# Kernel optimization log

Hardware: AMD Instinct MI355X
Metric: run time of the kernel (lower is better)

## Reference

```python
import jax, jax.numpy as jnp
import numpy as np

GAMMA = 0.997
N_STEPS = 5
EPS = 1e-3
Q_WEIGHTS = np.array([1.0, 0.5, 0.0, 2.0], dtype=np.float32)


def _rescale(x):
    # sign(x) * (sqrt(|x|+1) - 1) + eps * x
    return jnp.sign(x) * (jnp.sqrt(jnp.abs(x) + 1.0) - 1.0) + EPS * x


def _inv_rescale(x):
    sign = jnp.sign(x)
    sqrt_arg = 1.0 + 4.0 * EPS * (jnp.abs(x) + 1.0 + EPS)
    square = ((jnp.sqrt(sqrt_arg) - 1.0) / (2.0 * EPS)) ** 2
    return sign * (square - 1.0)


def setup_inputs() -> dict:
    key = jax.random.key(0)
    ks = jax.random.split(key, 6)
    B, T, Q = 4096, 512, 4
    current_q_value = jax.random.normal(ks[0], (B, T, Q), dtype=jnp.float32)
    next_q_value = jax.random.normal(ks[1], (B, T, Q), dtype=jnp.float32)
    log_p = jax.random.normal(ks[2], (B, T), dtype=jnp.float32)
    reward = jax.random.normal(ks[3], (B, T, Q), dtype=jnp.float32)
    is_done = jax.random.bernoulli(ks[4], 0.02, (B, T)).astype(jnp.float32)
    mask = jax.random.bernoulli(ks[5], 0.95, (B, T)).astype(jnp.float32)
    return {
        "current_q_value": current_q_value,
        "next_q_value": next_q_value,
        "log_p": log_p,
        "reward": reward,
        "is_done": is_done,
        "mask": mask,
    }


def reference(current_q_value, next_q_value, log_p, reward, is_done, mask):
    B, T, Q = reward.shape
    q_w = jnp.asarray(Q_WEIGHTS)[None, None, :]                     # (1,1,Q)
    nz = (q_w != 0)
    inv_qw = jnp.where(nz, 1.0 / jnp.where(nz, q_w, 1.0), 0.0)      # (1,1,Q)
    inv_num_q = 1.0 / float((Q_WEIGHTS != 0).sum())

    m = mask[..., None]                                             # (B,T,1)
    d = is_done[..., None]                                          # (B,T,1)

    nq = m * (1.0 - d) * _inv_rescale(next_q_value)                 # (B,T,Q)
    lp = inv_num_q * inv_qw * (m * (1.0 - d) * log_p[..., None])    # (B,T,Q)

    pad = jnp.zeros((B, N_STEPS - 1, Q), dtype=reward.dtype)
    pad_reward = jnp.concatenate([m * reward, pad], axis=1)         # (B,T+n-1,Q)
    lp_pad = jnp.concatenate([lp, pad], axis=1)                     # (B,T+n-1,Q)

    gpow = GAMMA ** jnp.arange(N_STEPS, dtype=jnp.float32)          # gamma^0..gamma^{n-1}
    widx = jnp.arange(T)[:, None] + jnp.arange(N_STEPS)[None, :]    # (T,n) window indices

    reward_sum = jnp.einsum('btnq,n->btq', pad_reward[:, widx, :], gpow)
    log_p_sum = jnp.einsum('btnq,n->btq', lp_pad[:, widx, :], gpow * GAMMA)

    idxs = jnp.minimum(T - 1, jnp.arange(T) + N_STEPS - 1)          # (T,)
    # NOTE: original code uses gamma**idx (absolute index), reproduced faithfully
    next_term = (GAMMA ** idxs.astype(jnp.float32))[None, :, None] * nq[:, idxs, :]

    target = _rescale(reward_sum + next_term + log_p_sum)           # (B,T,Q)
    loss = 0.5 * m * q_w * (current_q_value - target) ** 2
    return loss
```

## Files before the change

kernel.cpp:

```cpp
#include <hip/hip_runtime.h>
#include <math.h>

#define T_DIM 512
#define GAMMA_F 0.997f
#define EPS_F 1e-3f
#define LOG2_GAMMA (-0.0043345907f)

typedef float v4f __attribute__((ext_vector_type(4)));

__device__ __forceinline__ float inv_rescale_f(float x) {
    float s = (x > 0.f) ? 1.f : ((x < 0.f) ? -1.f : 0.f);
    float sqrt_arg = 1.f + 4.f * EPS_F * (fabsf(x) + 1.f + EPS_F);
    float q = (sqrtf(sqrt_arg) - 1.f) * (1.f / (2.f * EPS_F));
    return s * (q * q - 1.f);
}

__device__ __forceinline__ float rescale_f(float x) {
    return copysignf(sqrtf(fabsf(x) + 1.f) - 1.f, x) + EPS_F * x;
}

__global__ __launch_bounds__(256) void nstep_qloss_kernel(
    const float* __restrict__ cur_q,
    const float* __restrict__ next_q,
    const float* __restrict__ log_p,
    const float* __restrict__ reward,
    const float* __restrict__ is_done,
    const float* __restrict__ mask,
    float* __restrict__ out,
    int BT)
{
    int idx = blockIdx.x * 256 + threadIdx.x;
    if (idx >= BT) return;
    int t = idx & (T_DIM - 1);
    int base = idx - t;

    int s1 = (t + 1 < T_DIM) ? t + 1 : T_DIM - 1;
    int s2 = (t + 2 < T_DIM) ? t + 2 : T_DIM - 1;
    int s3 = (t + 3 < T_DIM) ? t + 3 : T_DIM - 1;
    int s4 = (t + 4 < T_DIM) ? t + 4 : T_DIM - 1;
    int o0 = idx;
    int o1 = base + s1, o2 = base + s2, o3 = base + s3, o4 = base + s4;

    const v4f* rew4 = (const v4f*)reward;
    const v4f* nq4  = (const v4f*)next_q;
    const v4f* cq4  = (const v4f*)cur_q;
    v4f* out4       = (v4f*)out;

    float m0 = mask[o0], m1 = mask[o1], m2 = mask[o2], m3 = mask[o3], m4 = mask[o4];
    float d0 = is_done[o0], d1 = is_done[o1], d2 = is_done[o2], d3 = is_done[o3], d4 = is_done[o4];
    float p0 = log_p[o0], p1 = log_p[o1], p2 = log_p[o2], p3 = log_p[o3], p4 = log_p[o4];
    v4f r0 = rew4[o0], r1 = rew4[o1], r2 = rew4[o2], r3 = rew4[o3], r4 = rew4[o4];
    v4f nq = nq4[o4];
    v4f cq = cq4[o0];

    float v1 = (t + 1 < T_DIM) ? 1.f : 0.f;
    float v2 = (t + 2 < T_DIM) ? 1.f : 0.f;
    float v3 = (t + 3 < T_DIM) ? 1.f : 0.f;
    float v4v = (t + 4 < T_DIM) ? 1.f : 0.f;

    const float g1 = GAMMA_F;
    const float g2 = g1 * g1;
    const float g3 = g2 * g1;
    const float g4 = g2 * g2;

    float w0 = m0;
    float w1 = v1 * g1 * m1;
    float w2 = v2 * g2 * m2;
    float w3 = v3 * g3 * m3;
    float w4 = v4v * g4 * m4;

    float a0 = w0 * r0.x; float a1 = w0 * r0.y; float a2 = w0 * r0.z; float a3 = w0 * r0.w;
    a0 = fmaf(w1, r1.x, a0); a1 = fmaf(w1, r1.y, a1); a2 = fmaf(w1, r1.z, a2); a3 = fmaf(w1, r1.w, a3);
    a0 = fmaf(w2, r2.x, a0); a1 = fmaf(w2, r2.y, a1); a2 = fmaf(w2, r2.z, a2); a3 = fmaf(w2, r2.w, a3);
    a0 = fmaf(w3, r3.x, a0); a1 = fmaf(w3, r3.y, a1); a2 = fmaf(w3, r3.z, a2); a3 = fmaf(w3, r3.w, a3);
    a0 = fmaf(w4, r4.x, a0); a1 = fmaf(w4, r4.y, a1); a2 = fmaf(w4, r4.z, a2); a3 = fmaf(w4, r4.w, a3);

    float Ls = w0 * (1.f - d0) * p0;
    Ls = fmaf(w1, (1.f - d1) * p1, Ls);
    Ls = fmaf(w2, (1.f - d2) * p2, Ls);
    Ls = fmaf(w3, (1.f - d3) * p3, Ls);
    Ls = fmaf(w4, (1.f - d4) * p4, Ls);
    Ls *= GAMMA_F * (1.f / 3.f);

    float coeff = exp2f((float)s4 * LOG2_GAMMA);
    float g = coeff * m4 * (1.f - d4);
    float nt0 = g * inv_rescale_f(nq.x);
    float nt1 = g * inv_rescale_f(nq.y);
    float nt2 = g * inv_rescale_f(nq.z);
    float nt3 = g * inv_rescale_f(nq.w);

    float tgt0 = rescale_f(a0 + nt0 + 1.0f * Ls);
    float tgt1 = rescale_f(a1 + nt1 + 2.0f * Ls);
    float tgt2 = rescale_f(a2 + nt2);
    float tgt3 = rescale_f(a3 + nt3 + 0.5f * Ls);

    float hm = 0.5f * m0;
    float e0 = cq.x - tgt0;
    float e1 = cq.y - tgt1;
    float e3 = cq.w - tgt3;
    (void)tgt2;
    v4f o;
    o.x = hm * e0 * e0;
    o.y = hm * 0.5f * e1 * e1;
    o.z = 0.f;
    o.w = hm * 2.0f * e3 * e3;
    out4[idx] = o;
}

extern "C" void kernel_launch(void* const* d_in, const int* in_sizes, int n_in,
                              void* d_out, int out_size, void* d_ws, size_t ws_size,
                              hipStream_t stream) {
    const float* cur_q   = (const float*)d_in[0];
    const float* next_q  = (const float*)d_in[1];
    const float* log_p   = (const float*)d_in[2];
    const float* reward  = (const float*)d_in[3];
    const float* is_done = (const float*)d_in[4];
    const float* mask    = (const float*)d_in[5];
    float* out = (float*)d_out;

    int BT = in_sizes[2];
    int blocks = (BT + 255) / 256;
    hipLaunchKernelGGL(nstep_qloss_kernel, dim3(blocks), dim3(256), 0, stream,
                       cur_q, next_q, log_p, reward, is_done, mask, out, BT);
}
```

Before: 157.7 us.

## Stage masked rewards and log-probs in shared memory for window reuse

Each thread now loads only its own timestep's mask, done flag, log_p and reward, precomputes the masked values, and writes them to shared memory with a four-element halo. Neighbouring timesteps in the 5-step window are then read from LDS instead of being reloaded from global memory five times. This removes redundant global and L2 traffic at the cost of a block barrier and about 6 KB of LDS per block. The bounds check is dropped and the grid uses BT/256, which assumes BT is a multiple of 256.

```diff
diff --git a/kernel.cpp b/kernel.cpp
--- a/kernel.cpp
+++ b/kernel.cpp
@@ -29,61 +29,91 @@
     float* __restrict__ out,
     int BT)
 {
-    int idx = blockIdx.x * 256 + threadIdx.x;
-    if (idx >= BT) return;
-    int t = idx & (T_DIM - 1);
+    __shared__ float s_md [260];
+    __shared__ float s_Lmd[260];
+    __shared__ float s_rx [260];
+    __shared__ float s_ry [260];
+    __shared__ float s_rz [260];
+    __shared__ float s_rw [260];
+
+    int tid = threadIdx.x;
+    int idx = blockIdx.x * 256 + tid;
+    int t   = idx & (T_DIM - 1);
     int base = idx - t;
-
-    int s1 = (t + 1 < T_DIM) ? t + 1 : T_DIM - 1;
-    int s2 = (t + 2 < T_DIM) ? t + 2 : T_DIM - 1;
-    int s3 = (t + 3 < T_DIM) ? t + 3 : T_DIM - 1;
-    int s4 = (t + 4 < T_DIM) ? t + 4 : T_DIM - 1;
-    int o0 = idx;
-    int o1 = base + s1, o2 = base + s2, o3 = base + s3, o4 = base + s4;
 
     const v4f* rew4 = (const v4f*)reward;
     const v4f* nq4  = (const v4f*)next_q;
     const v4f* cq4  = (const v4f*)cur_q;
     v4f* out4       = (v4f*)out;
 
-    float m0 = mask[o0], m1 = mask[o1], m2 = mask[o2], m3 = mask[o3], m4 = mask[o4];
-    float d0 = is_done[o0], d1 = is_done[o1], d2 = is_done[o2], d3 = is_done[o3], d4 = is_done[o4];
-    float p0 = log_p[o0], p1 = log_p[o1], p2 = log_p[o2], p3 = log_p[o3], p4 = log_p[o4];
-    v4f r0 = rew4[o0], r1 = rew4[o1], r2 = rew4[o2], r3 = rew4[o3], r4 = rew4[o4];
-    v4f nq = nq4[o4];
-    v4f cq = cq4[o0];
+    float m0 = mask[idx];
+    float d0 = is_done[idx];
+    float p0 = log_p[idx];
+    v4f   r  = rew4[idx];
+
+    int s4 = (t + 4 < T_DIM) ? t + 4 : T_DIM - 1;
+    v4f nq = nq4[base + s4];
+    v4f cq = cq4[idx];
+
+    float md0  = m0 * (1.f - d0);
+    float Lmd0 = md0 * p0;
+    float rx0 = m0 * r.x, ry0 = m0 * r.y, rz0 = m0 * r.z, rw0 = m0 * r.w;
+    s_md [tid] = md0;
+    s_Lmd[tid] = Lmd0;
+    s_rx [tid] = rx0;
+    s_ry [tid] = ry0;
+    s_rz [tid] = rz0;
+    s_rw [tid] = rw0;
+
+    if (tid < 4) {
+        int th = t + 256;
+        if (th > T_DIM - 1) th = T_DIM - 1;
+        int oh = base + th;
+        float mh = mask[oh];
+        float dh = is_done[oh];
+        float ph = log_p[oh];
+        v4f   rh = rew4[oh];
+        float mdh = mh * (1.f - dh);
+        s_md [256 + tid] = mdh;
+        s_Lmd[256 + tid] = mdh * ph;
+        s_rx [256 + tid] = mh * rh.x;
+        s_ry [256 + tid] = mh * rh.y;
+        s_rz [256 + tid] = mh * rh.z;
+        s_rw [256 + tid] = mh * rh.w;
+    }
+    __syncthreads();
 
     float v1 = (t + 1 < T_DIM) ? 1.f : 0.f;
     float v2 = (t + 2 < T_DIM) ? 1.f : 0.f;
     float v3 = (t + 3 < T_DIM) ? 1.f : 0.f;
-    float v4v = (t + 4 < T_DIM) ? 1.f : 0.f;
+    float v4 = (t + 4 < T_DIM) ? 1.f : 0.f;
 
     const float g1 = GAMMA_F;
     const float g2 = g1 * g1;
     const float g3 = g2 * g1;
     const float g4 = g2 * g2;
+    float w1 = v1 * g1, w2 = v2 * g2, w3 = v3 * g3, w4 = v4 * g4;
 
-    float w0 = m0;
-    float w1 = v1 * g1 * m1;
-    float w2 = v2 * g2 * m2;
-    float w3 = v3 * g3 * m3;
-    float w4 = v4v * g4 * m4;
+    float a0 = rx0, a1 = ry0, a2 = rz0, a3 = rw0;
+    a0 = fmaf(w1, s_rx[tid + 1], a0); a1 = fmaf(w1, s_ry[tid + 1], a1);
+    a2 = fmaf(w1, s_rz[tid + 1], a2); a3 = fmaf(w1, s_rw[tid + 1], a3);
+    a0 = fmaf(w2, s_rx[tid + 2], a0); a1 = fmaf(w2, s_ry[tid + 2], a1);
+    a2 = fmaf(w2, s_rz[tid + 2], a2); a3 = fmaf(w2, s_rw[tid + 2], a3);
+    a0 = fmaf(w3, s_rx[tid + 3], a0); a1 = fmaf(w3, s_ry[tid + 3], a1);
+    a2 = fmaf(w3, s_rz[tid + 3], a2); a3 = fmaf(w3, s_rw[tid + 3], a3);
+    a0 = fmaf(w4, s_rx[tid + 4], a0); a1 = fmaf(w4, s_ry[tid + 4], a1);
+    a2 = fmaf(w4, s_rz[tid + 4], a2); a3 = fmaf(w4, s_rw[tid + 4], a3);
 
-    float a0 = w0 * r0.x; float a1 = w0 * r0.y; float a2 = w0 * r0.z; float a3 = w0 * r0.w;
-    a0 = fmaf(w1, r1.x, a0); a1 = fmaf(w1, r1.y, a1); a2 = fmaf(w1, r1.z, a2); a3 = fmaf(w1, r1.w, a3);
-    a0 = fmaf(w2, r2.x, a0); a1 = fmaf(w2, r2.y, a1); a2 = fmaf(w2, r2.z, a2); a3 = fmaf(w2, r2.w, a3);
-    a0 = fmaf(w3, r3.x, a0); a1 = fmaf(w3, r3.y, a1); a2 = fmaf(w3, r3.z, a2); a3 = fmaf(w3, r3.w, a3);
-    a0 = fmaf(w4, r4.x, a0); a1 = fmaf(w4, r4.y, a1); a2 = fmaf(w4, r4.z, a2); a3 = fmaf(w4, r4.w, a3);
-
-    float Ls = w0 * (1.f - d0) * p0;
-    Ls = fmaf(w1, (1.f - d1) * p1, Ls);
-    Ls = fmaf(w2, (1.f - d2) * p2, Ls);
-    Ls = fmaf(w3, (1.f - d3) * p3, Ls);
-    Ls = fmaf(w4, (1.f - d4) * p4, Ls);
+    float Ls = Lmd0;
+    Ls = fmaf(w1, s_Lmd[tid + 1], Ls);
+    Ls = fmaf(w2, s_Lmd[tid + 2], Ls);
+    Ls = fmaf(w3, s_Lmd[tid + 3], Ls);
+    Ls = fmaf(w4, s_Lmd[tid + 4], Ls);
     Ls *= GAMMA_F * (1.f / 3.f);
 
+    float md4 = s_md[tid + 4];
     float coeff = exp2f((float)s4 * LOG2_GAMMA);
-    float g = coeff * m4 * (1.f - d4);
+    float g = coeff * md4;
     float nt0 = g * inv_rescale_f(nq.x);
     float nt1 = g * inv_rescale_f(nq.y);
     float nt2 = g * inv_rescale_f(nq.z);
@@ -93,18 +123,20 @@
     float tgt1 = rescale_f(a1 + nt1 + 2.0f * Ls);
     float tgt2 = rescale_f(a2 + nt2);
     float tgt3 = rescale_f(a3 + nt3 + 0.5f * Ls);
+    (void)tgt2;
 
     float hm = 0.5f * m0;
     float e0 = cq.x - tgt0;
     float e1 = cq.y - tgt1;
     float e3 = cq.w - tgt3;
-    (void)tgt2;
     v4f o;
     o.x = hm * e0 * e0;
     o.y = hm * 0.5f * e1 * e1;
     o.z = 0.f;
     o.w = hm * 2.0f * e3 * e3;
     out4[idx] = o;
+
+    (void)BT;
 }
 
 extern "C" void kernel_launch(void* const* d_in, const int* in_sizes, int n_in,
@@ -119,7 +151,7 @@
     float* out = (float*)d_out;
 
     int BT = in_sizes[2];
-    int blocks = (BT + 255) / 256;
+    int blocks = BT / 256;
     hipLaunchKernelGGL(nstep_qloss_kernel, dim3(blocks), dim3(256), 0, stream,
                        cur_q, next_q, log_p, reward, is_done, mask, out, BT);
 }
```

Measured after the change: 161.1 us. 2.1% more time.

## Stage windowed inputs in LDS and process four rows per block

Applied to the files above, without the earlier changes.

Each thread used to issue five overlapping gathers of mask, done, log_p and reward to build the 5-step window. The kernel now loads each element once into shared memory, with a small halo, and reads the window neighbours from LDS. Each block also handles four batch rows, so each thread has more independent loads in flight. This should cut redundant global and L2 traffic, since the kernel is memory-bound. The costs are a barrier, extra LDS traffic, and a grid that assumes B is divisible by 4 and T equals 512.

```diff
diff --git a/kernel.cpp b/kernel.cpp
--- a/kernel.cpp
+++ b/kernel.cpp
@@ -5,6 +5,8 @@
 #define GAMMA_F 0.997f
 #define EPS_F 1e-3f
 #define LOG2_GAMMA (-0.0043345907f)
+#define ROWS_PER_BLOCK 4
+#define TILE_T 256
 
 typedef float v4f __attribute__((ext_vector_type(4)));
 
@@ -19,92 +21,140 @@
     return copysignf(sqrtf(fabsf(x) + 1.f) - 1.f, x) + EPS_F * x;
 }
 
-__global__ __launch_bounds__(256) void nstep_qloss_kernel(
+#define LDS_STRIDE 260
+__global__ __launch_bounds__(256, 2) void nstep_qloss_kernel(
     const float* __restrict__ cur_q,
     const float* __restrict__ next_q,
     const float* __restrict__ log_p,
     const float* __restrict__ reward,
     const float* __restrict__ is_done,
     const float* __restrict__ mask,
-    float* __restrict__ out,
-    int BT)
+    float* __restrict__ out)
 {
-    int idx = blockIdx.x * 256 + threadIdx.x;
-    if (idx >= BT) return;
-    int t = idx & (T_DIM - 1);
-    int base = idx - t;
+    __shared__ float s_md [ROWS_PER_BLOCK * LDS_STRIDE];
+    __shared__ float s_Lmd[ROWS_PER_BLOCK * LDS_STRIDE];
+    __shared__ float s_rx [ROWS_PER_BLOCK * LDS_STRIDE];
+    __shared__ float s_ry [ROWS_PER_BLOCK * LDS_STRIDE];
+    __shared__ float s_rz [ROWS_PER_BLOCK * LDS_STRIDE];
+    __shared__ float s_rw [ROWS_PER_BLOCK * LDS_STRIDE];
 
-    int s1 = (t + 1 < T_DIM) ? t + 1 : T_DIM - 1;
-    int s2 = (t + 2 < T_DIM) ? t + 2 : T_DIM - 1;
-    int s3 = (t + 3 < T_DIM) ? t + 3 : T_DIM - 1;
-    int s4 = (t + 4 < T_DIM) ? t + 4 : T_DIM - 1;
-    int o0 = idx;
-    int o1 = base + s1, o2 = base + s2, o3 = base + s3, o4 = base + s4;
+    int tid  = threadIdx.x;
+    int tile = blockIdx.x & (T_DIM / TILE_T - 1);
+    int rgrp = blockIdx.x >> 1;
+    int t0   = tile * TILE_T;
+    int t    = t0 + tid;
+    int base0 = rgrp * ROWS_PER_BLOCK * T_DIM;
 
     const v4f* rew4 = (const v4f*)reward;
     const v4f* nq4  = (const v4f*)next_q;
     const v4f* cq4  = (const v4f*)cur_q;
     v4f* out4       = (v4f*)out;
 
-    float m0 = mask[o0], m1 = mask[o1], m2 = mask[o2], m3 = mask[o3], m4 = mask[o4];
-    float d0 = is_done[o0], d1 = is_done[o1], d2 = is_done[o2], d3 = is_done[o3], d4 = is_done[o4];
-    float p0 = log_p[o0], p1 = log_p[o1], p2 = log_p[o2], p3 = log_p[o3], p4 = log_p[o4];
-    v4f r0 = rew4[o0], r1 = rew4[o1], r2 = rew4[o2], r3 = rew4[o3], r4 = rew4[o4];
-    v4f nq = nq4[o4];
-    v4f cq = cq4[o0];
+    int s4 = (t + 4 < T_DIM) ? t + 4 : T_DIM - 1;
 
-    float v1 = (t + 1 < T_DIM) ? 1.f : 0.f;
-    float v2 = (t + 2 < T_DIM) ? 1.f : 0.f;
-    float v3 = (t + 3 < T_DIM) ? 1.f : 0.f;
-    float v4v = (t + 4 < T_DIM) ? 1.f : 0.f;
+    float m0[4], d0[4], p0[4];
+    v4f   r[4], nq[4], cq[4];
+#pragma unroll
+    for (int k = 0; k < ROWS_PER_BLOCK; ++k) {
+        int idx = base0 + k * T_DIM + t;
+        m0[k] = mask[idx];
+        d0[k] = is_done[idx];
+        p0[k] = log_p[idx];
+        r[k]  = rew4[idx];
+    }
+#pragma unroll
+    for (int k = 0; k < ROWS_PER_BLOCK; ++k) {
+        int rowb = base0 + k * T_DIM;
+        nq[k] = nq4[rowb + s4];
+        cq[k] = cq4[rowb + t];
+    }
+
+#pragma unroll
+    for (int k = 0; k < ROWS_PER_BLOCK; ++k) {
+        float md = m0[k] * (1.f - d0[k]);
+        int o = k * LDS_STRIDE + tid;
+        s_md [o] = md;
+        s_Lmd[o] = md * p0[k];
+        s_rx [o] = m0[k] * r[k].x;
+        s_ry [o] = m0[k] * r[k].y;
+        s_rz [o] = m0[k] * r[k].z;
+        s_rw [o] = m0[k] * r[k].w;
+    }
+
+    if (tid < 4 * ROWS_PER_BLOCK) {
+        int k = tid >> 2;
+        int j = tid & 3;
+        int th = t0 + TILE_T + j;
+        if (th > T_DIM - 1) th = T_DIM - 1;
+        int oh = base0 + k * T_DIM + th;
+        float mh = mask[oh];
+        float dh = is_done[oh];
+        float ph = log_p[oh];
+        v4f   rh = rew4[oh];
+        float mdh = mh * (1.f - dh);
+        int o = k * LDS_STRIDE + TILE_T + j;
+        s_md [o] = mdh;
+        s_Lmd[o] = mdh * ph;
+        s_rx [o] = mh * rh.x;
+        s_ry [o] = mh * rh.y;
+        s_rz [o] = mh * rh.z;
+        s_rw [o] = mh * rh.w;
+    }
+    __syncthreads();
 
     const float g1 = GAMMA_F;
     const float g2 = g1 * g1;
     const float g3 = g2 * g1;
     const float g4 = g2 * g2;
+    float w1 = ((t + 1 < T_DIM) ? 1.f : 0.f) * g1;
+    float w2 = ((t + 2 < T_DIM) ? 1.f : 0.f) * g2;
+    float w3 = ((t + 3 < T_DIM) ? 1.f : 0.f) * g3;
+    float w4 = ((t + 4 < T_DIM) ? 1.f : 0.f) * g4;
+    float coeff = exp2f((float)s4 * LOG2_GAMMA);
 
-    float w0 = m0;
-    float w1 = v1 * g1 * m1;
-    float w2 = v2 * g2 * m2;
-    float w3 = v3 * g3 * m3;
-    float w4 = v4v * g4 * m4;
+#pragma unroll
+    for (int k = 0; k < ROWS_PER_BLOCK; ++k) {
+        int o = k * LDS_STRIDE + tid;
+        float a0 = s_rx[o], a1 = s_ry[o], a2 = s_rz[o], a3 = s_rw[o];
+        a0 = fmaf(w1, s_rx[o + 1], a0); a1 = fmaf(w1, s_ry[o + 1], a1);
+        a2 = fmaf(w1, s_rz[o + 1], a2); a3 = fmaf(w1, s_rw[o + 1], a3);
+        a0 = fmaf(w2, s_rx[o + 2], a0); a1 = fmaf(w2, s_ry[o + 2], a1);
+        a2 = fmaf(w2, s_rz[o + 2], a2); a3 = fmaf(w2, s_rw[o + 2], a3);
+        a0 = fmaf(w3, s_rx[o + 3], a0); a1 = fmaf(w3, s_ry[o + 3], a1);
+        a2 = fmaf(w3, s_rz[o + 3], a2); a3 = fmaf(w3, s_rw[o + 3], a3);
+        a0 = fmaf(w4, s_rx[o + 4], a0); a1 = fmaf(w4, s_ry[o + 4], a1);
+        a2 = fmaf(w4, s_rz[o + 4], a2); a3 = fmaf(w4, s_rw[o + 4], a3);
 
-    float a0 = w0 * r0.x; float a1 = w0 * r0.y; float a2 = w0 * r0.z; float a3 = w0 * r0.w;
-    a0 = fmaf(w1, r1.x, a0); a1 = fmaf(w1, r1.y, a1); a2 = fmaf(w1, r1.z, a2); a3 = fmaf(w1, r1.w, a3);
-    a0 = fmaf(w2, r2.x, a0); a1 = fmaf(w2, r2.y, a1); a2 = fmaf(w2, r2.z, a2); a3 = fmaf(w2, r2.w, a3);
-    a0 = fmaf(w3, r3.x, a0); a1 = fmaf(w3, r3.y, a1); a2 = fmaf(w3, r3.z, a2); a3 = fmaf(w3, r3.w, a3);
-    a0 = fmaf(w4, r4.x, a0); a1 = fmaf(w4, r4.y, a1); a2 = fmaf(w4, r4.z, a2); a3 = fmaf(w4, r4.w, a3);
+        float Ls = s_Lmd[o];
+        Ls = fmaf(w1, s_Lmd[o + 1], Ls);
+        Ls = fmaf(w2, s_Lmd[o + 2], Ls);
+        Ls = fmaf(w3, s_Lmd[o + 3], Ls);
+        Ls = fmaf(w4, s_Lmd[o + 4], Ls);
+        Ls *= GAMMA_F * (1.f / 3.f);
 
-    float Ls = w0 * (1.f - d0) * p0;
-    Ls = fmaf(w1, (1.f - d1) * p1, Ls);
-    Ls = fmaf(w2, (1.f - d2) * p2, Ls);
-    Ls = fmaf(w3, (1.f - d3) * p3, Ls);
-    Ls = fmaf(w4, (1.f - d4) * p4, Ls);
-    Ls *= GAMMA_F * (1.f / 3.f);
+        float g = coeff * s_md[o + 4];
+        float nt0 = g * inv_rescale_f(nq[k].x);
+        float nt1 = g * inv_rescale_f(nq[k].y);
+        float nt2 = g * inv_rescale_f(nq[k].z);
+        float nt3 = g * inv_rescale_f(nq[k].w);
 
-    float coeff = exp2f((float)s4 * LOG2_GAMMA);
-    float g = coeff * m4 * (1.f - d4);
-    float nt0 = g * inv_rescale_f(nq.x);
-    float nt1 = g * inv_rescale_f(nq.y);
-    float nt2 = g * inv_rescale_f(nq.z);
-    float nt3 = g * inv_rescale_f(nq.w);
+        float tgt0 = rescale_f(a0 + nt0 + 1.0f * Ls);
+        float tgt1 = rescale_f(a1 + nt1 + 2.0f * Ls);
+        float tgt2 = rescale_f(a2 + nt2);
+        float tgt3 = rescale_f(a3 + nt3 + 0.5f * Ls);
+        (void)tgt2;
 
-    float tgt0 = rescale_f(a0 + nt0 + 1.0f * Ls);
-    float tgt1 = rescale_f(a1 + nt1 + 2.0f * Ls);
-    float tgt2 = rescale_f(a2 + nt2);
-    float tgt3 = rescale_f(a3 + nt3 + 0.5f * Ls);
-
-    float hm = 0.5f * m0;
-    float e0 = cq.x - tgt0;
-    float e1 = cq.y - tgt1;
-    float e3 = cq.w - tgt3;
-    (void)tgt2;
-    v4f o;
-    o.x = hm * e0 * e0;
-    o.y = hm * 0.5f * e1 * e1;
-    o.z = 0.f;
-    o.w = hm * 2.0f * e3 * e3;
-    out4[idx] = o;
+        float hm = 0.5f * m0[k];
+        float e0 = cq[k].x - tgt0;
+        float e1 = cq[k].y - tgt1;
+        float e3 = cq[k].w - tgt3;
+        v4f ov;
+        ov.x = hm * e0 * e0;
+        ov.y = hm * 0.5f * e1 * e1;
+        ov.z = 0.f;
+        ov.w = hm * 2.0f * e3 * e3;
+        out4[base0 + k * T_DIM + t] = ov;
+    }
 }
 
 extern "C" void kernel_launch(void* const* d_in, const int* in_sizes, int n_in,
@@ -119,7 +169,8 @@
     float* out = (float*)d_out;
 
     int BT = in_sizes[2];
-    int blocks = (BT + 255) / 256;
+    int B = BT / T_DIM;
+    int blocks = (T_DIM / TILE_T) * (B / ROWS_PER_BLOCK);
     hipLaunchKernelGGL(nstep_qloss_kernel, dim3(blocks), dim3(256), 0, stream,
-                       cur_q, next_q, log_p, reward, is_done, mask, out, BT);
+                       cur_q, next_q, log_p, reward, is_done, mask, out);
 }
```

New measurement: 164.0 us. 1.04x slower.

## Process four grid-strided chunks per thread with double-buffered register prefetch

Applied to the files above, without the earlier changes.

Each thread now handles four elements spaced one grid-stride apart. It loads the next chunk's inputs into a second register set while computing the current one, and the grid is a quarter the size. The goal is more memory-level parallelism and fewer blocks to schedule in a bandwidth-bound elementwise kernel. The cost is higher register pressure, with launch bounds asking for 4 blocks per CU. The bounds check is gone, so this assumes BT divides evenly by 1024, which holds for the given shape.

```diff
diff --git a/kernel.cpp b/kernel.cpp
--- a/kernel.cpp
+++ b/kernel.cpp
@@ -5,6 +5,7 @@
 #define GAMMA_F 0.997f
 #define EPS_F 1e-3f
 #define LOG2_GAMMA (-0.0043345907f)
+#define ITERS 4
 
 typedef float v4f __attribute__((ext_vector_type(4)));
 
@@ -19,7 +20,7 @@
     return copysignf(sqrtf(fabsf(x) + 1.f) - 1.f, x) + EPS_F * x;
 }
 
-__global__ __launch_bounds__(256) void nstep_qloss_kernel(
+__global__ __launch_bounds__(256, 4) void nstep_qloss_kernel(
     const float* __restrict__ cur_q,
     const float* __restrict__ next_q,
     const float* __restrict__ log_p,
@@ -27,84 +28,105 @@
     const float* __restrict__ is_done,
     const float* __restrict__ mask,
     float* __restrict__ out,
-    int BT)
+    int stride_elems)
 {
-    int idx = blockIdx.x * 256 + threadIdx.x;
-    if (idx >= BT) return;
-    int t = idx & (T_DIM - 1);
-    int base = idx - t;
+    int tid0 = blockIdx.x * 256 + threadIdx.x;
+    int t = tid0 & (T_DIM - 1);
+    int base = tid0 - t;
 
-    int s1 = (t + 1 < T_DIM) ? t + 1 : T_DIM - 1;
-    int s2 = (t + 2 < T_DIM) ? t + 2 : T_DIM - 1;
-    int s3 = (t + 3 < T_DIM) ? t + 3 : T_DIM - 1;
-    int s4 = (t + 4 < T_DIM) ? t + 4 : T_DIM - 1;
-    int o0 = idx;
-    int o1 = base + s1, o2 = base + s2, o3 = base + s3, o4 = base + s4;
+    int c0 = t;
+    int c1 = (t + 1 < T_DIM) ? t + 1 : T_DIM - 1;
+    int c2 = (t + 2 < T_DIM) ? t + 2 : T_DIM - 1;
+    int c3 = (t + 3 < T_DIM) ? t + 3 : T_DIM - 1;
+    int c4 = (t + 4 < T_DIM) ? t + 4 : T_DIM - 1;
+
+    const float g1 = GAMMA_F;
+    const float g2 = g1 * g1;
+    const float g3 = g2 * g1;
+    const float g4 = g2 * g2;
+    float w1c = ((t + 1 < T_DIM) ? 1.f : 0.f) * g1;
+    float w2c = ((t + 2 < T_DIM) ? 1.f : 0.f) * g2;
+    float w3c = ((t + 3 < T_DIM) ? 1.f : 0.f) * g3;
+    float w4c = ((t + 4 < T_DIM) ? 1.f : 0.f) * g4;
+    float coeff = exp2f((float)c4 * LOG2_GAMMA);
 
     const v4f* rew4 = (const v4f*)reward;
     const v4f* nq4  = (const v4f*)next_q;
     const v4f* cq4  = (const v4f*)cur_q;
     v4f* out4       = (v4f*)out;
 
-    float m0 = mask[o0], m1 = mask[o1], m2 = mask[o2], m3 = mask[o3], m4 = mask[o4];
-    float d0 = is_done[o0], d1 = is_done[o1], d2 = is_done[o2], d3 = is_done[o3], d4 = is_done[o4];
-    float p0 = log_p[o0], p1 = log_p[o1], p2 = log_p[o2], p3 = log_p[o3], p4 = log_p[o4];
-    v4f r0 = rew4[o0], r1 = rew4[o1], r2 = rew4[o2], r3 = rew4[o3], r4 = rew4[o4];
-    v4f nq = nq4[o4];
-    v4f cq = cq4[o0];
+    float m[2][5], d[2][5], p[2][5];
+    v4f   r[2][5], nqv[2], cqv[2];
 
-    float v1 = (t + 1 < T_DIM) ? 1.f : 0.f;
-    float v2 = (t + 2 < T_DIM) ? 1.f : 0.f;
-    float v3 = (t + 3 < T_DIM) ? 1.f : 0.f;
-    float v4v = (t + 4 < T_DIM) ? 1.f : 0.f;
+    auto LOADSET = [&](int s, int rb) {
+        m[s][0] = mask[rb + c0]; m[s][1] = mask[rb + c1]; m[s][2] = mask[rb + c2];
+        m[s][3] = mask[rb + c3]; m[s][4] = mask[rb + c4];
+        d[s][0] = is_done[rb + c0]; d[s][1] = is_done[rb + c1]; d[s][2] = is_done[rb + c2];
+        d[s][3] = is_done[rb + c3]; d[s][4] = is_done[rb + c4];
+        p[s][0] = log_p[rb + c0]; p[s][1] = log_p[rb + c1]; p[s][2] = log_p[rb + c2];
+        p[s][3] = log_p[rb + c3]; p[s][4] = log_p[rb + c4];
+        r[s][0] = rew4[rb + c0]; r[s][1] = rew4[rb + c1]; r[s][2] = rew4[rb + c2];
+        r[s][3] = rew4[rb + c3]; r[s][4] = rew4[rb + c4];
+        nqv[s] = nq4[rb + c4];
+        cqv[s] = cq4[rb + c0];
+    };
 
-    const float g1 = GAMMA_F;
-    const float g2 = g1 * g1;
-    const float g3 = g2 * g1;
-    const float g4 = g2 * g2;
+    auto COMPUTE = [&](int s, int rb) {
+        float w0 = m[s][0];
+        float w1 = w1c * m[s][1];
+        float w2 = w2c * m[s][2];
+        float w3 = w3c * m[s][3];
+        float w4 = w4c * m[s][4];
 
-    float w0 = m0;
-    float w1 = v1 * g1 * m1;
-    float w2 = v2 * g2 * m2;
-    float w3 = v3 * g3 * m3;
-    float w4 = v4v * g4 * m4;
+        float a0 = w0 * r[s][0].x, a1 = w0 * r[s][0].y, a2 = w0 * r[s][0].z, a3 = w0 * r[s][0].w;
+        a0 = fmaf(w1, r[s][1].x, a0); a1 = fmaf(w1, r[s][1].y, a1);
+        a2 = fmaf(w1, r[s][1].z, a2); a3 = fmaf(w1, r[s][1].w, a3);
+        a0 = fmaf(w2, r[s][2].x, a0); a1 = fmaf(w2, r[s][2].y, a1);
+        a2 = fmaf(w2, r[s][2].z, a2); a3 = fmaf(w2, r[s][2].w, a3);
+        a0 = fmaf(w3, r[s][3].x, a0); a1 = fmaf(w3, r[s][3].y, a1);
+        a2 = fmaf(w3, r[s][3].z, a2); a3 = fmaf(w3, r[s][3].w, a3);
+        a0 = fmaf(w4, r[s][4].x, a0); a1 = fmaf(w4, r[s][4].y, a1);
+        a2 = fmaf(w4, r[s][4].z, a2); a3 = fmaf(w4, r[s][4].w, a3);
 
-    float a0 = w0 * r0.x; float a1 = w0 * r0.y; float a2 = w0 * r0.z; float a3 = w0 * r0.w;
-    a0 = fmaf(w1, r1.x, a0); a1 = fmaf(w1, r1.y, a1); a2 = fmaf(w1, r1.z, a2); a3 = fmaf(w1, r1.w, a3);
-    a0 = fmaf(w2, r2.x, a0); a1 = fmaf(w2, r2.y, a1); a2 = fmaf(w2, r2.z, a2); a3 = fmaf(w2, r2.w, a3);
-    a0 = fmaf(w3, r3.x, a0); a1 = fmaf(w3, r3.y, a1); a2 = fmaf(w3, r3.z, a2); a3 = fmaf(w3, r3.w, a3);
-    a0 = fmaf(w4, r4.x, a0); a1 = fmaf(w4, r4.y, a1); a2 = fmaf(w4, r4.z, a2); a3 = fmaf(w4, r4.w, a3);
+        float Ls = w0 * (1.f - d[s][0]) * p[s][0];
+        Ls = fmaf(w1, (1.f - d[s][1]) * p[s][1], Ls);
+        Ls = fmaf(w2, (1.f - d[s][2]) * p[s][2], Ls);
+        Ls = fmaf(w3, (1.f - d[s][3]) * p[s][3], Ls);
+        Ls = fmaf(w4, (1.f - d[s][4]) * p[s][4], Ls);
+        Ls *= GAMMA_F * (1.f / 3.f);
 
-    float Ls = w0 * (1.f - d0) * p0;
-    Ls = fmaf(w1, (1.f - d1) * p1, Ls);
-    Ls = fmaf(w2, (1.f - d2) * p2, Ls);
-    Ls = fmaf(w3, (1.f - d3) * p3, Ls);
-    Ls = fmaf(w4, (1.f - d4) * p4, Ls);
-    Ls *= GAMMA_F * (1.f / 3.f);
+        float g = coeff * m[s][4] * (1.f - d[s][4]);
+        float nt0 = g * inv_rescale_f(nqv[s].x);
+        float nt1 = g * inv_rescale_f(nqv[s].y);
+        float nt2 = g * inv_rescale_f(nqv[s].z);
+        float nt3 = g * inv_rescale_f(nqv[s].w);
 
-    float coeff = exp2f((float)s4 * LOG2_GAMMA);
-    float g = coeff * m4 * (1.f - d4);
-    float nt0 = g * inv_rescale_f(nq.x);
-    float nt1 = g * inv_rescale_f(nq.y);
-    float nt2 = g * inv_rescale_f(nq.z);
-    float nt3 = g * inv_rescale_f(nq.w);
+        float tgt0 = rescale_f(a0 + nt0 + 1.0f * Ls);
+        float tgt1 = rescale_f(a1 + nt1 + 2.0f * Ls);
+        float tgt2 = rescale_f(a2 + nt2);
+        float tgt3 = rescale_f(a3 + nt3 + 0.5f * Ls);
+        (void)tgt2;
 
-    float tgt0 = rescale_f(a0 + nt0 + 1.0f * Ls);
-    float tgt1 = rescale_f(a1 + nt1 + 2.0f * Ls);
-    float tgt2 = rescale_f(a2 + nt2);
-    float tgt3 = rescale_f(a3 + nt3 + 0.5f * Ls);
+        float hm = 0.5f * m[s][0];
+        float e0 = cqv[s].x - tgt0;
+        float e1 = cqv[s].y - tgt1;
+        float e3 = cqv[s].w - tgt3;
+        v4f o;
+        o.x = hm * e0 * e0;
+        o.y = hm * 0.5f * e1 * e1;
+        o.z = 0.f;
+        o.w = hm * 2.0f * e3 * e3;
+        out4[rb + t] = o;
+    };
 
-    float hm = 0.5f * m0;
-    float e0 = cq.x - tgt0;
-    float e1 = cq.y - tgt1;
-    float e3 = cq.w - tgt3;
-    (void)tgt2;
-    v4f o;
-    o.x = hm * e0 * e0;
-    o.y = hm * 0.5f * e1 * e1;
-    o.z = 0.f;
-    o.w = hm * 2.0f * e3 * e3;
-    out4[idx] = o;
+    LOADSET(0, base);
+#pragma unroll
+    for (int i = 0; i < ITERS; ++i) {
+        int rb = base + i * stride_elems;
+        if (i + 1 < ITERS)
+            LOADSET((i + 1) & 1, rb + stride_elems);
+        COMPUTE(i & 1, rb);
+    }
 }
 
 extern "C" void kernel_launch(void* const* d_in, const int* in_sizes, int n_in,
@@ -119,7 +141,8 @@
     float* out = (float*)d_out;
 
     int BT = in_sizes[2];
-    int blocks = (BT + 255) / 256;
+    int blocks = BT / (256 * ITERS);
+    int stride_elems = blocks * 256;
     hipLaunchKernelGGL(nstep_qloss_kernel, dim3(blocks), dim3(256), 0, stream,
-                       cur_q, next_q, log_p, reward, is_done, mask, out, BT);
+                       cur_q, next_q, log_p, reward, is_done, mask, out, stride_elems);
 }
```

Result: slower. 162.0 us (+2.7%).
